# Kernel optimization log

Measured on AMD Instinct MI355X. Metric: run time of the kernel, lower is better.

Reference implementation:

```python
import jax, jax.numpy as jnp
import numpy as np

N_NODES = 50000
N_EDGES = 600000
HID = 128
OUT = 14
LAYERS = 3
N_GRAPHS = 16
NODE_VOCAB = (120, 6)
EDGE_VOCAB = (6, 3)
GEN_EPS = 1e-7   # GENConv eps added after ReLU on messages
BN_EPS = 1e-5    # torch BatchNorm1d default eps


def setup_inputs() -> dict:
    key = jax.random.key(0)
    ks = jax.random.split(key, 14)
    inp = {}
    inp['node_feat0'] = jax.random.randint(ks[0], (N_NODES,), 0, NODE_VOCAB[0], dtype=jnp.int32)
    inp['node_feat1'] = jax.random.randint(ks[1], (N_NODES,), 0, NODE_VOCAB[1], dtype=jnp.int32)
    inp['edge_feat0'] = jax.random.randint(ks[2], (N_EDGES,), 0, EDGE_VOCAB[0], dtype=jnp.int32)
    inp['edge_feat1'] = jax.random.randint(ks[3], (N_EDGES,), 0, EDGE_VOCAB[1], dtype=jnp.int32)
    inp['edge_src'] = jax.random.randint(ks[4], (N_EDGES,), 0, N_NODES, dtype=jnp.int32)
    inp['edge_dst'] = jax.random.randint(ks[5], (N_EDGES,), 0, N_NODES, dtype=jnp.int32)
    inp['graph_ids'] = jnp.repeat(jnp.arange(N_GRAPHS, dtype=jnp.int32), N_NODES // N_GRAPHS)
    inp['num_graphs'] = N_GRAPHS
    s = 0.05
    inp['W_node0'] = jax.random.normal(ks[6], (NODE_VOCAB[0], HID), jnp.float32) * s
    inp['W_node1'] = jax.random.normal(ks[7], (NODE_VOCAB[1], HID), jnp.float32) * s
    # per-layer edge embedding tables (each GENConv layer has its own)
    inp['edge_emb0'] = jax.random.normal(ks[8], (LAYERS, EDGE_VOCAB[0], HID), jnp.float32) * s
    inp['edge_emb1'] = jax.random.normal(ks[9], (LAYERS, EDGE_VOCAB[1], HID), jnp.float32) * s
    inp['beta'] = jnp.ones((LAYERS,), jnp.float32)  # learnable softmax temperature, init 1.0
    inp['mlp_W'] = jax.random.normal(ks[10], (LAYERS, HID, HID), jnp.float32) * (1.0 / np.sqrt(HID))
    inp['mlp_b'] = jnp.zeros((LAYERS, HID), jnp.float32)
    inp['bn_gamma'] = jnp.ones((LAYERS, HID), jnp.float32)
    inp['bn_beta'] = jnp.zeros((LAYERS, HID), jnp.float32)
    inp['W_out'] = jax.random.normal(ks[11], (HID, OUT), jnp.float32) * (1.0 / np.sqrt(HID))
    inp['b_out'] = jnp.zeros((OUT,), jnp.float32)
    return inp


def _segment_softmax(z, seg, num_segments):
    # DGL edge_softmax: elementwise softmax over edges sharing a destination node.
    zmax = jax.ops.segment_max(z, seg, num_segments=num_segments)
    zmax = jnp.where(jnp.isfinite(zmax), zmax, 0.0)  # guard empty segments
    e = jnp.exp(z - zmax[seg])
    denom = jax.ops.segment_sum(e, seg, num_segments=num_segments)
    return e / denom[seg]


def reference(node_feat0, node_feat1, edge_feat0, edge_feat1, edge_src, edge_dst,
              graph_ids, num_graphs, W_node0, W_node1, edge_emb0, edge_emb1,
              beta, mlp_W, mlp_b, bn_gamma, bn_beta, W_out, b_out):
    # node embedding lookup + sum over tables
    hv = W_node0[node_feat0] + W_node1[node_feat1]          # [N, H]
    n = hv.shape[0]
    for l in range(mlp_W.shape[0]):
        # BatchNorm1d (training mode: batch stats, biased variance) + ReLU
        mu = jnp.mean(hv, axis=0)
        var = jnp.var(hv, axis=0)
        hv1 = (hv - mu) * jax.lax.rsqrt(var + BN_EPS) * bn_gamma[l] + bn_beta[l]
        hv1 = jax.nn.relu(hv1)
        # GENConv: edge embed sum, u_add_e, relu+eps, edge_softmax, scatter-sum
        ee = edge_emb0[l][edge_feat0] + edge_emb1[l][edge_feat1]   # [E, H]
        m = jax.nn.relu(hv1[edge_src] + ee) + GEN_EPS              # [E, H]
        a = _segment_softmax(m * beta[l], edge_dst, n)             # [E, H]
        agg = jax.ops.segment_sum(m * a, edge_dst, num_segments=n)  # [N, H]
        # feats = node_feats + msg, then 1-layer MLP, then outer skip connect
        hv = (hv1 + agg) @ mlp_W[l] + mlp_b[l] + hv
    # AvgPooling over each graph in the batch, then output Linear
    counts = jax.ops.segment_sum(jnp.ones((n,), hv.dtype), graph_ids, num_segments=num_graphs)
    hg = jax.ops.segment_sum(hv, graph_ids, num_segments=num_graphs) / counts[:, None]
    return hg @ W_out + b_out  # [num_graphs, OUT]
```

## Files before the change

### kernel.cpp

```cpp
#include <hip/hip_runtime.h>

#define N_NODESC 50000
#define N_EDGESC 600000
#define HID 128
#define LAYERS 3
#define N_GRAPHSC 16
#define OUT_DIM 14
#define GEN_EPS 1e-7f
#define BN_EPS 1e-5f
#define SCAN_BLK 196
#define EMB_BLK 6250
#define WF_BLK 192
#define CNT_BLK 2344
#define GEMM_BLK 782
#define BNR_BLK 64
#define LOG2E 1.44269504f

typedef short bf16x8 __attribute__((ext_vector_type(8)));
typedef float f32x4 __attribute__((ext_vector_type(4)));

__device__ __forceinline__ unsigned short f2bf(float f) {
    union { float f; unsigned u; } v; v.f = f;
    unsigned r = v.u + 0x7FFF + ((v.u >> 16) & 1);
    return (unsigned short)(r >> 16);
}
__device__ __forceinline__ float bf_lo(unsigned u) {
    return __uint_as_float(u << 16);
}
__device__ __forceinline__ float bf_hi(unsigned u) {
    return __uint_as_float(u & 0xFFFF0000u);
}
__device__ __forceinline__ float bfs(unsigned short u) {
    return __uint_as_float(((unsigned)u) << 16);
}

__global__ void k_blocksum(const int* __restrict__ deg, int* __restrict__ part) {
    __shared__ int sh[256];
    int t = threadIdx.x;
    int i = blockIdx.x * 256 + t;
    sh[t] = (i < N_NODESC) ? deg[i] : 0;
    __syncthreads();
    for (int off = 128; off > 0; off >>= 1) {
        if (t < off) sh[t] += sh[t + off];
        __syncthreads();
    }
    if (t == 0) part[blockIdx.x] = sh[0];
}

__global__ void k_scanpart(const int* __restrict__ part, int* __restrict__ bofs) {
    __shared__ int sh[256];
    int t = threadIdx.x;
    int v = (t < SCAN_BLK) ? part[t] : 0;
    sh[t] = v;
    __syncthreads();
    for (int off = 1; off < 256; off <<= 1) {
        int add = (t >= off) ? sh[t - off] : 0;
        __syncthreads();
        sh[t] += add;
        __syncthreads();
    }
    if (t < SCAN_BLK) bofs[t] = sh[t] - v;
}

__global__ void k_rowptr(const int* __restrict__ deg, const int* __restrict__ bofs,
                         int* __restrict__ row_ptr, int* __restrict__ cursor) {
    __shared__ int sh[256];
    int t = threadIdx.x;
    int i = blockIdx.x * 256 + t;
    int d = (i < N_NODESC) ? deg[i] : 0;
    sh[t] = d;
    __syncthreads();
    for (int off = 1; off < 256; off <<= 1) {
        int add = (t >= off) ? sh[t - off] : 0;
        __syncthreads();
        sh[t] += add;
        __syncthreads();
    }
    if (i < N_NODESC) {
        int rp = bofs[blockIdx.x] + sh[t] - d;
        row_ptr[i] = rp;
        cursor[i] = rp;
    }
    if (i == 0) row_ptr[N_NODESC] = N_EDGESC;
}

__global__ void k_scatter(const int* __restrict__ dst, const int* __restrict__ src,
                          const int* __restrict__ f0, const int* __restrict__ f1,
                          int* __restrict__ cursor, int* __restrict__ csr_pack) {
    int i = blockIdx.x * blockDim.x + threadIdx.x;
    if (i < N_EDGESC) {
        int pos = atomicAdd(&cursor[dst[i]], 1);
        csr_pack[pos] = (src[i] << 8) | ((f0[i] * 3 + f1[i]) * 8);
    }
}

__global__ void k_embed(const int* __restrict__ f0, const int* __restrict__ f1,
                        const float4* __restrict__ W0, const float4* __restrict__ W1,
                        uint2* __restrict__ hvb2, float* __restrict__ part,
                        const float* __restrict__ W, unsigned short* __restrict__ wf,
                        const int* __restrict__ edst, int* __restrict__ deg) {
    int tid = threadIdx.x;
    if (blockIdx.x >= EMB_BLK + WF_BLK) {
        int e = (blockIdx.x - EMB_BLK - WF_BLK) * 256 + tid;
        if (e < N_EDGESC) atomicAdd(&deg[edst[e]], 1);
        return;
    }
    if (blockIdx.x >= EMB_BLK) {
        int i = (blockIdx.x - EMB_BLK) * 256 + tid;
        if (i < LAYERS * 16384) {
            int j = i & 7;
            int lane = (i >> 3) & 63;
            int nt = (i >> 9) & 7;
            int ks = (i >> 12) & 3;
            int l = i >> 14;
            int k = ks * 32 + (lane >> 4) * 8 + j;
            int n = nt * 16 + (lane & 15);
            wf[i] = f2bf(W[(size_t)l * HID * HID + k * HID + n]);
        }
        return;
    }
    __shared__ float sh[1024], sh2[1024];
    int i = blockIdx.x * 256 + tid;
    int v = i >> 5, c4 = i & 31;
    float4 a = W0[f0[v] * 32 + c4];
    float4 b = W1[f1[v] * 32 + c4];
    float4 o = make_float4(a.x + b.x, a.y + b.y, a.z + b.z, a.w + b.w);
    uint2 ob;
    ob.x = (unsigned)f2bf(o.x) | ((unsigned)f2bf(o.y) << 16);
    ob.y = (unsigned)f2bf(o.z) | ((unsigned)f2bf(o.w) << 16);
    hvb2[i] = ob;
    sh[tid * 4 + 0] = o.x; sh2[tid * 4 + 0] = o.x * o.x;
    sh[tid * 4 + 1] = o.y; sh2[tid * 4 + 1] = o.y * o.y;
    sh[tid * 4 + 2] = o.z; sh2[tid * 4 + 2] = o.z * o.z;
    sh[tid * 4 + 3] = o.w; sh2[tid * 4 + 3] = o.w * o.w;
    __syncthreads();
    if (tid < 128) {
        int c4i = tid >> 2, j = tid & 3;
        float s = 0.f, s2 = 0.f;
#pragma unroll
        for (int r = 0; r < 8; r++) {
            s += sh[(r * 32 + c4i) * 4 + j];
            s2 += sh2[(r * 32 + c4i) * 4 + j];
        }
        part[(size_t)blockIdx.x * 256 + tid] = s;
        part[(size_t)blockIdx.x * 256 + 128 + tid] = s2;
    }
}

__global__ void k_bn_reduce2(const float* __restrict__ part, int nparts,
                             float* __restrict__ gsum) {
    int t = threadIdx.x;
    int rows = (nparts + BNR_BLK - 1) / BNR_BLK;
    int r0 = blockIdx.x * rows;
    int r1 = min(r0 + rows, nparts);
    float s = 0.f;
    for (int p = r0; p < r1; p++) s += part[(size_t)p * 256 + t];
    atomicAdd(&gsum[t], s);
}

__global__ __launch_bounds__(512) void k_aggemm(
    const unsigned* __restrict__ hin, unsigned short* __restrict__ hout,
    const int* __restrict__ row_ptr, const int* __restrict__ csr_pack,
    const float* __restrict__ e0, const float* __restrict__ e1,
    const float* __restrict__ beta_p, const unsigned short* __restrict__ wf,
    const float* __restrict__ b, const float* __restrict__ gsum,
    const float* __restrict__ gamma, const float* __restrict__ betab,
    float* __restrict__ gsum_next, float* __restrict__ hg) {
    __shared__ float2 sh_et[18 * 64];
    __shared__ unsigned x_tile[64 * 64];
    __shared__ float shs[512], shs2[512];
    int tid = threadIdx.x;
    for (int i = tid; i < 18 * 64; i += 512) {
        int f = i >> 6, ln = i & 63;
        int a = f / 3, bb = f - 3 * a;
        float2 ea = *(const float2*)(e0 + a * HID + 2 * ln);
        float2 eb = *(const float2*)(e1 + bb * HID + 2 * ln);
        sh_et[i] = make_float2(ea.x + eb.x, ea.y + eb.y);
    }
    int w = tid >> 6, lane = tid & 63;
    int m0 = blockIdx.x * 64;
    const float bl2 = (*beta_p) * LOG2E;
    const float invN = 1.f / (float)N_NODESC;
    int cch = lane * 2;
    float mu0 = gsum[cch] * invN, mu1 = gsum[cch + 1] * invN;
    float var0 = gsum[128 + cch] * invN - mu0 * mu0;
    float var1 = gsum[129 + cch] * invN - mu1 * mu1;
    float sc0 = gamma[cch] * rsqrtf(var0 + BN_EPS);
    float sc1 = gamma[cch + 1] * rsqrtf(var1 + BN_EPS);
    float sf0 = betab[cch] - mu0 * sc0;
    float sf1 = betab[cch + 1] - mu1 * sc1;
    __syncthreads();

    const char* hinc = (const char*)hin;
    const char* etc = (const char*)sh_et;
    unsigned lane4 = (unsigned)lane * 4;
    unsigned lane8 = (unsigned)lane * 8;

#define AGG_BODY(J)                                                         \
    {                                                                       \
        int pack = __shfl(pk, (J), 64);                                     \
        unsigned u = *(const unsigned*)(hinc +                              \
                        ((((unsigned)pack) & 0xFFFFFF00u) + lane4));        \
        float2 t = *(const float2*)(etc +                                   \
                        (((((unsigned)pack) & 0xFFu) << 6) + lane8));       \
        float a0 = fmaxf(fmaf(bf_lo(u), sc0, sf0), 0.f);                    \
        float a1 = fmaxf(fmaf(bf_hi(u), sc1, sf1), 0.f);                    \
        float r0 = fmaxf(a0 + t.x, 0.f);                                    \
        float r1 = fmaxf(a1 + t.y, 0.f);                                    \
        float w0 = exp2f(r0 * bl2);                                         \
        float w1 = exp2f(r1 * bl2);                                         \
        d0 += w0; d1 += w1;                                                 \
        n0 = fmaf(r0, w0, n0); n1 = fmaf(r1, w1, n1);                       \
    }

    for (int i = 0; i < 8; i++) {
        int row = w * 8 + i;
        int v = m0 + row;
        int vc = min(v, N_NODESC - 1);
        unsigned su = hin[(size_t)vc * 64 + lane];
        float h10 = fmaxf(fmaf(bf_lo(su), sc0, sf0), 0.f);
        float h11 = fmaxf(fmaf(bf_hi(su), sc1, sf1), 0.f);
        int p0 = row_ptr[vc];
        int deg = (v < N_NODESC) ? (row_ptr[vc + 1] - p0) : 0;
        float n0 = 0.f, n1 = 0.f, d0 = 0.f, d1 = 0.f;
        for (int base = 0; base < deg; base += 64) {
            int idx = base + lane;
            int pk = (idx < deg) ? csr_pack[p0 + idx] : 0;
            int jn = min(64, deg - base);
            int j = 0;
            for (; j + 2 <= jn; j += 2) {
                AGG_BODY(j)
                AGG_BODY(j + 1)
            }
            if (j < jn) AGG_BODY(j)
        }
        float ox = h10 + (deg ? __fdividef(n0, d0) + GEN_EPS : 0.f);
        float oy = h11 + (deg ? __fdividef(n1, d1) + GEN_EPS : 0.f);
        x_tile[row * 64 + ((lane + row * 4) & 63)] =
            (unsigned)f2bf(ox) | ((unsigned)f2bf(oy) << 16);
    }
#undef AGG_BODY
    __syncthreads();

    int rw = w & 3, chh = w >> 2;
    int mrow = lane & 15, grp = lane >> 4;
    int rbase = rw * 16 + mrow;
    bf16x8 af[4];
#pragma unroll
    for (int ks = 0; ks < 4; ks++) {
        int col = ks * 16 + grp * 4;
        int colr = (col + rbase * 4) & 63;
        af[ks] = *(const bf16x8*)&x_tile[rbase * 64 + colr];
    }
    f32x4 acc[4];
#pragma unroll
    for (int nt = 0; nt < 4; nt++) acc[nt] = (f32x4){0.f, 0.f, 0.f, 0.f};
#pragma unroll
    for (int nt = 0; nt < 4; nt++) {
        int ntg = chh * 4 + nt;
#pragma unroll
        for (int ks = 0; ks < 4; ks++) {
            bf16x8 bfr = *(const bf16x8*)(wf +
                (size_t)((ks * 8 + ntg) * 64 + lane) * 8);
            acc[nt] = __builtin_amdgcn_mfma_f32_16x16x32_bf16(
                af[ks], bfr, acc[nt], 0, 0, 0);
        }
    }
    const unsigned short* hin_s = (const unsigned short*)hin;
    int gA = m0 / 3125;
    int boundary = (gA + 1) * 3125;
#pragma unroll
    for (int nt = 0; nt < 4; nt++) {
        int col = chh * 64 + nt * 16 + mrow;
        float bias = b[col];
        float s = 0.f, s2 = 0.f;
#pragma unroll
        for (int r = 0; r < 4; r++) {
            int v = m0 + rw * 16 + grp * 4 + r;
            if (v < N_NODESC) {
                size_t idx = (size_t)v * HID + col;
                float o = acc[nt][r] + bias + bfs(hin_s[idx]);
                hout[idx] = f2bf(o);
                if (hg) {
                    if (v < boundary) s += o; else s2 += o;
                } else {
                    s += o; s2 += o * o;
                }
            }
        }
        s  += __shfl_xor(s, 16, 64);  s  += __shfl_xor(s, 32, 64);
        s2 += __shfl_xor(s2, 16, 64); s2 += __shfl_xor(s2, 32, 64);
        if (lane < 16) { shs[rw * 128 + col] = s; shs2[rw * 128 + col] = s2; }
    }
    __syncthreads();
    if (hg) {
        int gB = min(m0 + 63, N_NODESC - 1) / 3125;
        if (tid < 128) {
            atomicAdd(&hg[gA * 128 + tid],
                shs[tid] + shs[128 + tid] + shs[256 + tid] + shs[384 + tid]);
        } else if (tid < 256 && gB != gA) {
            int c = tid - 128;
            atomicAdd(&hg[gB * 128 + c],
                shs2[c] + shs2[128 + c] + shs2[256 + c] + shs2[384 + c]);
        }
    } else if (gsum_next) {
        if (tid < 128) {
            atomicAdd(&gsum_next[tid],
                shs[tid] + shs[128 + tid] + shs[256 + tid] + shs[384 + tid]);
        } else if (tid < 256) {
            int c = tid - 128;
            atomicAdd(&gsum_next[tid],
                shs2[c] + shs2[128 + c] + shs2[256 + c] + shs2[384 + c]);
        }
    }
}

__global__ void k_finish(const float* __restrict__ hg, const float* __restrict__ Wo,
                         const float* __restrict__ bo, float* __restrict__ out) {
    int t = threadIdx.x;
    if (t >= N_GRAPHSC * OUT_DIM) return;
    int g = t / OUT_DIM, o = t % OUT_DIM;
    const float inv = (float)N_GRAPHSC / (float)N_NODESC;
    float acc = bo[o];
    for (int k = 0; k < HID; k++)
        acc += hg[g * HID + k] * inv * Wo[k * OUT_DIM + o];
    out[t] = acc;
}

extern "C" void kernel_launch(void* const* d_in, const int* in_sizes, int n_in,
                              void* d_out, int out_size, void* d_ws, size_t ws_size,
                              hipStream_t stream) {
    const int* node_feat0 = (const int*)d_in[0];
    const int* node_feat1 = (const int*)d_in[1];
    const int* edge_feat0 = (const int*)d_in[2];
    const int* edge_feat1 = (const int*)d_in[3];
    const int* edge_src   = (const int*)d_in[4];
    const int* edge_dst   = (const int*)d_in[5];
    const float* W_node0   = (const float*)d_in[8];
    const float* W_node1   = (const float*)d_in[9];
    const float* edge_emb0 = (const float*)d_in[10];
    const float* edge_emb1 = (const float*)d_in[11];
    const float* beta      = (const float*)d_in[12];
    const float* mlp_W     = (const float*)d_in[13];
    const float* mlp_b     = (const float*)d_in[14];
    const float* bn_gamma  = (const float*)d_in[15];
    const float* bn_beta   = (const float*)d_in[16];
    const float* W_out     = (const float*)d_in[17];
    const float* b_out     = (const float*)d_in[18];
    float* out = (float*)d_out;

    char* ws = (char*)d_ws;
    size_t off = 0;
    auto alloc = [&](size_t bytes) -> void* {
        void* p = ws + off;
        off += (bytes + 255) & ~(size_t)255;
        return p;
    };
    unsigned short* hvA = (unsigned short*)alloc((size_t)N_NODESC * HID * 2);
    unsigned short* hvB = (unsigned short*)alloc((size_t)N_NODESC * HID * 2);
    float* gsums   = (float*)alloc(LAYERS * 256 * 4);
    float* hg      = (float*)alloc(N_GRAPHSC * HID * 4);
    float* bnpart  = (float*)alloc((size_t)EMB_BLK * 256 * 4);
    unsigned short* wfrag = (unsigned short*)alloc((size_t)LAYERS * 16384 * 2);
    int* row_ptr   = (int*)alloc((N_NODESC + 1) * 4);
    int* cursor    = (int*)alloc(N_NODESC * 4);
    int* deg       = (int*)alloc(N_NODESC * 4);
    int* part      = (int*)alloc(SCAN_BLK * 4);
    int* bofs      = (int*)alloc(SCAN_BLK * 4);
    int* csr_pack  = (int*)alloc((size_t)N_EDGESC * 4);

    hipMemsetAsync(deg, 0, N_NODESC * 4, stream);
    hipMemsetAsync(gsums, 0, LAYERS * 256 * 4 + N_GRAPHSC * HID * 4, stream);

    k_embed<<<EMB_BLK + WF_BLK + CNT_BLK, 256, 0, stream>>>(
        node_feat0, node_feat1, (const float4*)W_node0, (const float4*)W_node1,
        (uint2*)hvA, bnpart, mlp_W, wfrag, edge_dst, deg);

    k_blocksum<<<SCAN_BLK, 256, 0, stream>>>(deg, part);
    k_scanpart<<<1, 256, 0, stream>>>(part, bofs);
    k_rowptr<<<SCAN_BLK, 256, 0, stream>>>(deg, bofs, row_ptr, cursor);
    k_scatter<<<(N_EDGESC + 255) / 256, 256, 0, stream>>>(
        edge_dst, edge_src, edge_feat0, edge_feat1, cursor, csr_pack);

    k_bn_reduce2<<<BNR_BLK, 256, 0, stream>>>(bnpart, EMB_BLK, gsums);

    unsigned short* hin = hvA;
    unsigned short* hout = hvB;
    for (int l = 0; l < LAYERS; l++) {
        float* gsum = gsums + l * 256;
        float* gnext = (l + 1 < LAYERS) ? gsums + (l + 1) * 256 : nullptr;
        float* hgp = (l == LAYERS - 1) ? hg : nullptr;
        k_aggemm<<<GEMM_BLK, 512, 0, stream>>>(
            (const unsigned*)hin, hout, row_ptr, csr_pack,
            edge_emb0 + (size_t)l * 6 * HID, edge_emb1 + (size_t)l * 3 * HID,
            beta + l, wfrag + (size_t)l * 16384, mlp_b + l * HID,
            gsum, bn_gamma + l * HID, bn_beta + l * HID, gnext, hgp);
        unsigned short* tmp = hin; hin = hout; hout = tmp;
    }

    k_finish<<<1, 256, 0, stream>>>(hg, W_out, b_out, out);
}
```

Before: 422.4 us.

## Fuse CSR scan kernels, merge BN reduce into scatter, fold finish into last layer

Replaces the three-kernel degree scan (blocksum, scanpart, rowptr) with a single decoupled-lookback scan kernel that uses a per-block status array. It merges the BN partial reduction into the edge scatter launch as extra blocks, folds the final output linear layer into the last aggregation kernel through a last-block counter, and collapses two memsets into one. The aim is to cut kernel launch count and the serialization gaps between small kernels. In exchange it relies on blocks being scheduled in order for the lookback spin-wait, and adds a threadfence and an atomic counter to the last layer.

```diff
diff --git a/kernel.cpp b/kernel.cpp
--- a/kernel.cpp
+++ b/kernel.cpp
@@ -8,12 +8,13 @@
 #define OUT_DIM 14
 #define GEN_EPS 1e-7f
 #define BN_EPS 1e-5f
-#define SCAN_BLK 196
+#define CSR_BLK 196
 #define EMB_BLK 6250
 #define WF_BLK 192
 #define CNT_BLK 2344
+#define SCT_BLK 2344
+#define BNR_BLK 64
 #define GEMM_BLK 782
-#define BNR_BLK 64
 #define LOG2E 1.44269504f
 
 typedef short bf16x8 __attribute__((ext_vector_type(8)));
@@ -32,66 +33,6 @@
 }
 __device__ __forceinline__ float bfs(unsigned short u) {
     return __uint_as_float(((unsigned)u) << 16);
-}
-
-__global__ void k_blocksum(const int* __restrict__ deg, int* __restrict__ part) {
-    __shared__ int sh[256];
-    int t = threadIdx.x;
-    int i = blockIdx.x * 256 + t;
-    sh[t] = (i < N_NODESC) ? deg[i] : 0;
-    __syncthreads();
-    for (int off = 128; off > 0; off >>= 1) {
-        if (t < off) sh[t] += sh[t + off];
-        __syncthreads();
-    }
-    if (t == 0) part[blockIdx.x] = sh[0];
-}
-
-__global__ void k_scanpart(const int* __restrict__ part, int* __restrict__ bofs) {
-    __shared__ int sh[256];
-    int t = threadIdx.x;
-    int v = (t < SCAN_BLK) ? part[t] : 0;
-    sh[t] = v;
-    __syncthreads();
-    for (int off = 1; off < 256; off <<= 1) {
-        int add = (t >= off) ? sh[t - off] : 0;
-        __syncthreads();
-        sh[t] += add;
-        __syncthreads();
-    }
-    if (t < SCAN_BLK) bofs[t] = sh[t] - v;
-}
-
-__global__ void k_rowptr(const int* __restrict__ deg, const int* __restrict__ bofs,
-                         int* __restrict__ row_ptr, int* __restrict__ cursor) {
-    __shared__ int sh[256];
-    int t = threadIdx.x;
-    int i = blockIdx.x * 256 + t;
-    int d = (i < N_NODESC) ? deg[i] : 0;
-    sh[t] = d;
-    __syncthreads();
-    for (int off = 1; off < 256; off <<= 1) {
-        int add = (t >= off) ? sh[t - off] : 0;
-        __syncthreads();
-        sh[t] += add;
-        __syncthreads();
-    }
-    if (i < N_NODESC) {
-        int rp = bofs[blockIdx.x] + sh[t] - d;
-        row_ptr[i] = rp;
-        cursor[i] = rp;
-    }
-    if (i == 0) row_ptr[N_NODESC] = N_EDGESC;
-}
-
-__global__ void k_scatter(const int* __restrict__ dst, const int* __restrict__ src,
-                          const int* __restrict__ f0, const int* __restrict__ f1,
-                          int* __restrict__ cursor, int* __restrict__ csr_pack) {
-    int i = blockIdx.x * blockDim.x + threadIdx.x;
-    if (i < N_EDGESC) {
-        int pos = atomicAdd(&cursor[dst[i]], 1);
-        csr_pack[pos] = (src[i] << 8) | ((f0[i] * 3 + f1[i]) * 8);
-    }
 }
 
 __global__ void k_embed(const int* __restrict__ f0, const int* __restrict__ f1,
@@ -147,15 +88,85 @@
     }
 }
 
-__global__ void k_bn_reduce2(const float* __restrict__ part, int nparts,
-                             float* __restrict__ gsum) {
-    int t = threadIdx.x;
-    int rows = (nparts + BNR_BLK - 1) / BNR_BLK;
-    int r0 = blockIdx.x * rows;
-    int r1 = min(r0 + rows, nparts);
-    float s = 0.f;
-    for (int p = r0; p < r1; p++) s += part[(size_t)p * 256 + t];
-    atomicAdd(&gsum[t], s);
+__global__ void k_csr(const int* __restrict__ deg,
+                      unsigned long long* __restrict__ status,
+                      int* __restrict__ row_ptr, int* __restrict__ cursor) {
+    __shared__ int sh[256];
+    __shared__ int s_prev;
+    int t = threadIdx.x, b = blockIdx.x;
+    int i = b * 256 + t;
+    int d = (i < N_NODESC) ? deg[i] : 0;
+    sh[t] = d;
+    __syncthreads();
+    for (int off = 1; off < 256; off <<= 1) {
+        int add = (t >= off) ? sh[t - off] : 0;
+        __syncthreads();
+        sh[t] += add;
+        __syncthreads();
+    }
+    int agg = sh[255];
+    if (t == 0) {
+        unsigned long long st0 =
+            ((unsigned long long)((b == 0) ? 2 : 1) << 32) | (unsigned)agg;
+        atomicExch(&status[b], st0);
+        if (b == 0) s_prev = 0;
+    }
+    if (b > 0 && t < 64) {
+        int run = 0;
+        int q = b - 1 - t;
+        for (;;) {
+            unsigned long long st;
+            if (q >= 0) {
+                do { st = atomicAdd(&status[q], 0ull); } while ((st >> 32) == 0);
+            } else {
+                st = (2ull << 32);
+            }
+            int isDone = ((st >> 32) == 2ull);
+            unsigned long long mask2 = __ballot(isDone);
+            int first2 = (int)__ffsll((long long)mask2) - 1;
+            int lim = (first2 >= 0) ? first2 : 63;
+            int contrib = (t <= lim) ? (int)(unsigned)(st & 0xFFFFFFFFull) : 0;
+#pragma unroll
+            for (int o = 1; o < 64; o <<= 1)
+                contrib += __shfl_xor(contrib, o, 64);
+            run += contrib;
+            if (first2 >= 0) break;
+            q -= 64;
+        }
+        if (t == 0) {
+            atomicExch(&status[b], (2ull << 32) | (unsigned)(run + agg));
+            s_prev = run;
+        }
+    }
+    __syncthreads();
+    if (i < N_NODESC) {
+        int rp = s_prev + sh[t] - d;
+        row_ptr[i] = rp;
+        cursor[i] = rp;
+    }
+    if (i == 0) row_ptr[N_NODESC] = N_EDGESC;
+}
+
+__global__ void k_scatter(const int* __restrict__ dst, const int* __restrict__ src,
+                          const int* __restrict__ f0, const int* __restrict__ f1,
+                          int* __restrict__ cursor, int* __restrict__ csr_pack,
+                          const float* __restrict__ part, float* __restrict__ gsum) {
+    int tid = threadIdx.x;
+    if (blockIdx.x >= SCT_BLK) {
+        int bb = blockIdx.x - SCT_BLK;
+        int rows = (EMB_BLK + BNR_BLK - 1) / BNR_BLK;
+        int r0 = bb * rows;
+        int r1 = min(r0 + rows, EMB_BLK);
+        float s = 0.f;
+        for (int p = r0; p < r1; p++) s += part[(size_t)p * 256 + tid];
+        atomicAdd(&gsum[tid], s);
+        return;
+    }
+    int i = blockIdx.x * 256 + tid;
+    if (i < N_EDGESC) {
+        int pos = atomicAdd(&cursor[dst[i]], 1);
+        csr_pack[pos] = (src[i] << 8) | ((f0[i] * 3 + f1[i]) * 8);
+    }
 }
 
 __global__ __launch_bounds__(512) void k_aggemm(
@@ -165,10 +176,13 @@
     const float* __restrict__ beta_p, const unsigned short* __restrict__ wf,
     const float* __restrict__ b, const float* __restrict__ gsum,
     const float* __restrict__ gamma, const float* __restrict__ betab,
-    float* __restrict__ gsum_next, float* __restrict__ hg) {
+    float* __restrict__ gsum_next, float* __restrict__ hg,
+    const float* __restrict__ Wo, const float* __restrict__ bo,
+    float* __restrict__ out, int* __restrict__ fctr) {
     __shared__ float2 sh_et[18 * 64];
     __shared__ unsigned x_tile[64 * 64];
     __shared__ float shs[512], shs2[512];
+    __shared__ int s_last;
     int tid = threadIdx.x;
     for (int i = tid; i < 18 * 64; i += 512) {
         int f = i >> 6, ln = i & 63;
@@ -303,6 +317,20 @@
             atomicAdd(&hg[gB * 128 + c],
                 shs2[c] + shs2[128 + c] + shs2[256 + c] + shs2[384 + c]);
         }
+        __threadfence();
+        if (tid == 0) s_last = atomicAdd(fctr, 1);
+        __syncthreads();
+        if (s_last == (int)gridDim.x - 1) {
+            __threadfence();
+            if (tid < N_GRAPHSC * OUT_DIM) {
+                int g = tid / OUT_DIM, o = tid % OUT_DIM;
+                const float inv = (float)N_GRAPHSC / (float)N_NODESC;
+                float acc2 = bo[o];
+                for (int k = 0; k < HID; k++)
+                    acc2 += hg[g * HID + k] * inv * Wo[k * OUT_DIM + o];
+                out[tid] = acc2;
+            }
+        }
     } else if (gsum_next) {
         if (tid < 128) {
             atomicAdd(&gsum_next[tid],
@@ -313,18 +341,6 @@
                 shs2[c] + shs2[128 + c] + shs2[256 + c] + shs2[384 + c]);
         }
     }
-}
-
-__global__ void k_finish(const float* __restrict__ hg, const float* __restrict__ Wo,
-                         const float* __restrict__ bo, float* __restrict__ out) {
-    int t = threadIdx.x;
-    if (t >= N_GRAPHSC * OUT_DIM) return;
-    int g = t / OUT_DIM, o = t % OUT_DIM;
-    const float inv = (float)N_GRAPHSC / (float)N_NODESC;
-    float acc = bo[o];
-    for (int k = 0; k < HID; k++)
-        acc += hg[g * HID + k] * inv * Wo[k * OUT_DIM + o];
-    out[t] = acc;
 }
 
 extern "C" void kernel_launch(void* const* d_in, const int* in_sizes, int n_in,
@@ -358,31 +374,29 @@
     };
     unsigned short* hvA = (unsigned short*)alloc((size_t)N_NODESC * HID * 2);
     unsigned short* hvB = (unsigned short*)alloc((size_t)N_NODESC * HID * 2);
-    float* gsums   = (float*)alloc(LAYERS * 256 * 4);
-    float* hg      = (float*)alloc(N_GRAPHSC * HID * 4);
     float* bnpart  = (float*)alloc((size_t)EMB_BLK * 256 * 4);
     unsigned short* wfrag = (unsigned short*)alloc((size_t)LAYERS * 16384 * 2);
     int* row_ptr   = (int*)alloc((N_NODESC + 1) * 4);
     int* cursor    = (int*)alloc(N_NODESC * 4);
-    int* deg       = (int*)alloc(N_NODESC * 4);
-    int* part      = (int*)alloc(SCAN_BLK * 4);
-    int* bofs      = (int*)alloc(SCAN_BLK * 4);
     int* csr_pack  = (int*)alloc((size_t)N_EDGESC * 4);
-
-    hipMemsetAsync(deg, 0, N_NODESC * 4, stream);
-    hipMemsetAsync(gsums, 0, LAYERS * 256 * 4 + N_GRAPHSC * HID * 4, stream);
+    int* deg = (int*)alloc(N_NODESC * 4);
+    unsigned long long* status = (unsigned long long*)alloc(CSR_BLK * 8);
+    float* gsums = (float*)alloc(LAYERS * 256 * 4);
+    float* hg    = (float*)alloc(N_GRAPHSC * HID * 4);
+    int* fctr    = (int*)alloc(256);
+    size_t zero_bytes = (size_t)(((char*)fctr + 256) - (char*)deg);
+
+    hipMemsetAsync(deg, 0, zero_bytes, stream);
 
     k_embed<<<EMB_BLK + WF_BLK + CNT_BLK, 256, 0, stream>>>(
         node_feat0, node_feat1, (const float4*)W_node0, (const float4*)W_node1,
         (uint2*)hvA, bnpart, mlp_W, wfrag, edge_dst, deg);
 
-    k_blocksum<<<SCAN_BLK, 256, 0, stream>>>(deg, part);
-    k_scanpart<<<1, 256, 0, stream>>>(part, bofs);
-    k_rowptr<<<SCAN_BLK, 256, 0, stream>>>(deg, bofs, row_ptr, cursor);
-    k_scatter<<<(N_EDGESC + 255) / 256, 256, 0, stream>>>(
-        edge_dst, edge_src, edge_feat0, edge_feat1, cursor, csr_pack);
-
-    k_bn_reduce2<<<BNR_BLK, 256, 0, stream>>>(bnpart, EMB_BLK, gsums);
+    k_csr<<<CSR_BLK, 256, 0, stream>>>(deg, status, row_ptr, cursor);
+
+    k_scatter<<<SCT_BLK + BNR_BLK, 256, 0, stream>>>(
+        edge_dst, edge_src, edge_feat0, edge_feat1, cursor, csr_pack,
+        bnpart, gsums);
 
     unsigned short* hin = hvA;
     unsigned short* hout = hvB;
@@ -394,9 +408,8 @@
             (const unsigned*)hin, hout, row_ptr, csr_pack,
             edge_emb0 + (size_t)l * 6 * HID, edge_emb1 + (size_t)l * 3 * HID,
             beta + l, wfrag + (size_t)l * 16384, mlp_b + l * HID,
-            gsum, bn_gamma + l * HID, bn_beta + l * HID, gnext, hgp);
+            gsum, bn_gamma + l * HID, bn_beta + l * HID, gnext, hgp,
+            W_out, b_out, out, fctr);
         unsigned short* tmp = hin; hin = hout; hout = tmp;
     }
-
-    k_finish<<<1, 256, 0, stream>>>(hg, W_out, b_out, out);
-}
+}
```

Result: slower. 559.3 us (+32.4%).
